# Kernel tuning notes

Hardware: AMD Instinct MI355X
Metric: run time of the kernel (lower is better)

The kernel has to match this reference:

```python
import jax, jax.numpy as jnp
import numpy as np

N_VIDEOS = 256
EMBED_DIM = 1024
MARGIN = 0.0

def _segment_sizes():
    i = np.arange(N_VIDEOS)
    num_clips = 8 + (i % 17)            # sum = 4088
    num_caps = 8 + ((5 * i + 3) % 17)   # sum = 4091
    return num_clips, num_caps

def setup_inputs() -> dict:
    key = jax.random.key(0)
    num_clips, num_caps = _segment_sizes()
    total_clips = int(num_clips.sum())
    total_caps = int(num_caps.sum())
    k1, k2 = jax.random.split(key)
    im = jax.random.normal(k1, (total_clips, EMBED_DIM), dtype=jnp.float32)
    s = jax.random.normal(k2, (total_caps, EMBED_DIM), dtype=jnp.float32)
    return {
        "im": im,
        "s": s,
        "num_clips": jnp.asarray(num_clips, jnp.int32),
        "num_caps": jnp.asarray(num_caps, jnp.int32),
    }

def reference(im, s, num_clips, num_caps):
    N = num_clips.shape[0]
    # full similarity matrix [total_clips, total_caps]
    scores = im @ s.T
    # segment ids mapping each clip/caption row to its video group
    clip_seg = jnp.repeat(jnp.arange(N), num_clips, total_repeat_length=im.shape[0])
    cap_seg = jnp.repeat(jnp.arange(N), num_caps, total_repeat_length=s.shape[0])
    # two-stage segmented sum -> block sums [N, N], then divide for block means
    row_red = jax.ops.segment_sum(scores, clip_seg, num_segments=N)       # [N, total_caps]
    blk_sum = jax.ops.segment_sum(row_red.T, cap_seg, num_segments=N).T   # [N, N]
    counts = num_clips.astype(jnp.float32)[:, None] * num_caps.astype(jnp.float32)[None, :]
    S = blk_sum / counts
    diag = jnp.diag(S)
    cost_s = jnp.maximum(MARGIN + S - diag[:, None], 0.0)   # caption retrieval
    cost_im = jnp.maximum(MARGIN + S - diag[None, :], 0.0)  # image retrieval
    eye = jnp.eye(N, dtype=bool)
    cost_s = jnp.where(eye, 0.0, cost_s)
    cost_im = jnp.where(eye, 0.0, cost_im)
    return cost_s.sum() + cost_im.sum()
```

## Files before the change

### kernel.cpp

```cpp
#include <hip/hip_runtime.h>
#include <hip/hip_bf16.h>

#define NVID 256
#define DIM 1024

typedef short bf16x8 __attribute__((ext_vector_type(8)));
typedef float f32x4 __attribute__((ext_vector_type(4)));

__device__ inline void acc4(float4& a, const float4& v) {
    a.x += v.x; a.y += v.y; a.z += v.z; a.w += v.w;
}

__device__ inline unsigned short f2bf(float f) {
    __hip_bfloat16 h = __float2bfloat16(f);
    unsigned short u;
    __builtin_memcpy(&u, &h, 2);
    return u;
}

__device__ inline float bf2f(unsigned short u) {
    return __uint_as_float(((unsigned)u) << 16);
}

__device__ inline float4 mean_rows(const float* __restrict__ src, int off, int n, int t) {
    const float4* srcv = (const float4*)src + (size_t)off * (DIM / 4) + t;
    float4 a0 = {0,0,0,0}, a1 = {0,0,0,0}, a2 = {0,0,0,0}, a3 = {0,0,0,0};
    int r = 0;
    for (; r + 8 <= n; r += 8) {
        float4 v0 = srcv[(size_t)(r + 0) * (DIM / 4)];
        float4 v1 = srcv[(size_t)(r + 1) * (DIM / 4)];
        float4 v2 = srcv[(size_t)(r + 2) * (DIM / 4)];
        float4 v3 = srcv[(size_t)(r + 3) * (DIM / 4)];
        float4 v4 = srcv[(size_t)(r + 4) * (DIM / 4)];
        float4 v5 = srcv[(size_t)(r + 5) * (DIM / 4)];
        float4 v6 = srcv[(size_t)(r + 6) * (DIM / 4)];
        float4 v7 = srcv[(size_t)(r + 7) * (DIM / 4)];
        acc4(a0, v0); acc4(a1, v1); acc4(a2, v2); acc4(a3, v3);
        acc4(a0, v4); acc4(a1, v5); acc4(a2, v6); acc4(a3, v7);
    }
    for (; r < n; ++r) acc4(a0, srcv[(size_t)r * (DIM / 4)]);
    acc4(a0, a1); acc4(a2, a3); acc4(a0, a2);
    const float inv = 1.0f / (float)n;
    a0.x *= inv; a0.y *= inv; a0.z *= inv; a0.w *= inv;
    return a0;
}

__global__ __launch_bounds__(256) void mean_diag_kernel(
    const float* __restrict__ im, const float* __restrict__ s,
    const int* __restrict__ num_clips, const int* __restrict__ num_caps,
    unsigned short* __restrict__ Ab, unsigned short* __restrict__ Bb,
    float* __restrict__ diag, float* __restrict__ out)
{
    const int i = blockIdx.x;
    const int t = threadIdx.x;
    if (i == 0 && t == 0) out[0] = 0.0f;

    __shared__ int sc[NVID], sp[NVID];
    sc[t] = num_clips[t];
    sp[t] = num_caps[t];
    __syncthreads();

    int offc = 0, offp = 0;
    for (int k = 0; k < i; ++k) { offc += sc[k]; offp += sp[k]; }
    const int nc = sc[i], np = sp[i];

    float4 am = mean_rows(im, offc, nc, t);
    float4 bm = mean_rows(s,  offp, np, t);

    ushort4 ua, ub;
    ua.x = f2bf(am.x); ua.y = f2bf(am.y); ua.z = f2bf(am.z); ua.w = f2bf(am.w);
    ub.x = f2bf(bm.x); ub.y = f2bf(bm.y); ub.z = f2bf(bm.z); ub.w = f2bf(bm.w);
    ((ushort4*)(Ab + (size_t)i * DIM))[t] = ua;
    ((ushort4*)(Bb + (size_t)i * DIM))[t] = ub;

    float p = bf2f(ua.x) * bf2f(ub.x) + bf2f(ua.y) * bf2f(ub.y)
            + bf2f(ua.z) * bf2f(ub.z) + bf2f(ua.w) * bf2f(ub.w);
    for (int o = 32; o > 0; o >>= 1) p += __shfl_down(p, o, 64);

    __shared__ float wsum[4];
    const int wave = t >> 6, lane = t & 63;
    if (lane == 0) wsum[wave] = p;
    __syncthreads();
    if (t == 0) diag[i] = wsum[0] + wsum[1] + wsum[2] + wsum[3];
}

__global__ __launch_bounds__(64) void loss_kernel(
    const unsigned short* __restrict__ Ab, const unsigned short* __restrict__ Bb,
    const float* __restrict__ diag, float* __restrict__ out)
{
    const int lane = threadIdx.x;
    const int i0 = blockIdx.y * 16, j0 = blockIdx.x * 16;
    const int m = lane & 15, q = lane >> 4;

    const unsigned short* Ap = Ab + (size_t)(i0 + m) * DIM + q * 8;
    const unsigned short* Bp = Bb + (size_t)(j0 + m) * DIM + q * 8;

    f32x4 acc = {0.f, 0.f, 0.f, 0.f};
#pragma unroll
    for (int kb = 0; kb < DIM; kb += 32) {
        bf16x8 a = *(const bf16x8*)(Ap + kb);
        bf16x8 b = *(const bf16x8*)(Bp + kb);
        acc = __builtin_amdgcn_mfma_f32_16x16x32_bf16(a, b, acc, 0, 0, 0);
    }

    const int j = j0 + m;
    const float dj = diag[j];
    const float4 di = *(const float4*)&diag[i0 + q * 4];
    const float dia[4] = {di.x, di.y, di.z, di.w};

    float v = 0.f;
#pragma unroll
    for (int r = 0; r < 4; ++r) {
        const int i = i0 + q * 4 + r;
        if (i != j) {
            const float sv = acc[r];
            v += fmaxf(sv - dia[r], 0.f) + fmaxf(sv - dj, 0.f);
        }
    }

    for (int o = 32; o > 0; o >>= 1) v += __shfl_down(v, o, 64);
    if (lane == 0) atomicAdd(out, v);
}

extern "C" void kernel_launch(void* const* d_in, const int* in_sizes, int n_in,
                              void* d_out, int out_size, void* d_ws, size_t ws_size,
                              hipStream_t stream) {
    const float* im    = (const float*)d_in[0];
    const float* s     = (const float*)d_in[1];
    const int*   nclip = (const int*)d_in[2];
    const int*   ncap  = (const int*)d_in[3];
    float* out = (float*)d_out;

    unsigned short* Ab = (unsigned short*)d_ws;
    unsigned short* Bb = Ab + NVID * DIM;
    float* diag = (float*)(Bb + NVID * DIM);

    mean_diag_kernel<<<NVID, 256, 0, stream>>>(im, s, nclip, ncap, Ab, Bb, diag, out);
    loss_kernel<<<dim3(16, 16), 64, 0, stream>>>(Ab, Bb, diag, out);
}
```

Before: 86.33 us.

## Split mean kernel across column halves and compute offsets via wave reduction

The mean/diag kernel now launches two blocks of 128 threads per video, each covering half of the embedding columns, so twice as many blocks spread across the CUs. The serial per-thread prefix loop over segment counts is replaced by a packed clip/caption count sum using a shuffle reduction. The diagonal is written as two partial sums that the loss kernel adds together. The packed 16-bit offsets assume the totals fit in 16 bits, which holds for these sizes.

```diff
diff --git a/kernel.cpp b/kernel.cpp
--- a/kernel.cpp
+++ b/kernel.cpp
@@ -22,8 +22,8 @@
     return __uint_as_float(((unsigned)u) << 16);
 }
 
-__device__ inline float4 mean_rows(const float* __restrict__ src, int off, int n, int t) {
-    const float4* srcv = (const float4*)src + (size_t)off * (DIM / 4) + t;
+__device__ inline float4 mean_rows_half(const float* __restrict__ src, int n, int t) {
+    const float4* srcv = (const float4*)src + t;
     float4 a0 = {0,0,0,0}, a1 = {0,0,0,0}, a2 = {0,0,0,0}, a3 = {0,0,0,0};
     int r = 0;
     for (; r + 8 <= n; r += 8) {
@@ -45,48 +45,60 @@
     return a0;
 }
 
-__global__ __launch_bounds__(256) void mean_diag_kernel(
+__global__ __launch_bounds__(128) void mean_diag_kernel(
     const float* __restrict__ im, const float* __restrict__ s,
     const int* __restrict__ num_clips, const int* __restrict__ num_caps,
     unsigned short* __restrict__ Ab, unsigned short* __restrict__ Bb,
-    float* __restrict__ diag, float* __restrict__ out)
+    float* __restrict__ diagp, float* __restrict__ out)
 {
-    const int i = blockIdx.x;
+    const int b = blockIdx.x;
     const int t = threadIdx.x;
-    if (i == 0 && t == 0) out[0] = 0.0f;
+    const int vid = b & (NVID - 1);
+    const int half = b >> 8;
+    if (b == 0 && t == 0) out[0] = 0.0f;
 
-    __shared__ int sc[NVID], sp[NVID];
-    sc[t] = num_clips[t];
-    sp[t] = num_caps[t];
+    int psum = 0;
+    {
+        int k0 = t, k1 = t + 128;
+        int v0 = num_clips[k0] | (num_caps[k0] << 16);
+        int v1 = num_clips[k1] | (num_caps[k1] << 16);
+        if (k0 < vid) psum += v0;
+        if (k1 < vid) psum += v1;
+    }
+    for (int o = 32; o > 0; o >>= 1) psum += __shfl_down(psum, o, 64);
+    __shared__ int wpart[2];
+    const int wave = t >> 6, lane = t & 63;
+    if (lane == 0) wpart[wave] = psum;
     __syncthreads();
+    const int packed = wpart[0] + wpart[1];
+    const int offc = packed & 0xFFFF;
+    const int offp = (packed >> 16) & 0xFFFF;
+    const int nc = num_clips[vid];
+    const int np = num_caps[vid];
 
-    int offc = 0, offp = 0;
-    for (int k = 0; k < i; ++k) { offc += sc[k]; offp += sp[k]; }
-    const int nc = sc[i], np = sp[i];
+    const int colBase = half * (DIM / 2);
 
-    float4 am = mean_rows(im, offc, nc, t);
-    float4 bm = mean_rows(s,  offp, np, t);
+    float4 am = mean_rows_half(im + (size_t)offc * DIM + colBase, nc, t);
+    float4 bm = mean_rows_half(s  + (size_t)offp * DIM + colBase, np, t);
 
     ushort4 ua, ub;
     ua.x = f2bf(am.x); ua.y = f2bf(am.y); ua.z = f2bf(am.z); ua.w = f2bf(am.w);
     ub.x = f2bf(bm.x); ub.y = f2bf(bm.y); ub.z = f2bf(bm.z); ub.w = f2bf(bm.w);
-    ((ushort4*)(Ab + (size_t)i * DIM))[t] = ua;
-    ((ushort4*)(Bb + (size_t)i * DIM))[t] = ub;
+    ((ushort4*)(Ab + (size_t)vid * DIM + colBase))[t] = ua;
+    ((ushort4*)(Bb + (size_t)vid * DIM + colBase))[t] = ub;
 
     float p = bf2f(ua.x) * bf2f(ub.x) + bf2f(ua.y) * bf2f(ub.y)
             + bf2f(ua.z) * bf2f(ub.z) + bf2f(ua.w) * bf2f(ub.w);
     for (int o = 32; o > 0; o >>= 1) p += __shfl_down(p, o, 64);
-
-    __shared__ float wsum[4];
-    const int wave = t >> 6, lane = t & 63;
+    __shared__ float wsum[2];
     if (lane == 0) wsum[wave] = p;
     __syncthreads();
-    if (t == 0) diag[i] = wsum[0] + wsum[1] + wsum[2] + wsum[3];
+    if (t == 0) diagp[half * NVID + vid] = wsum[0] + wsum[1];
 }
 
 __global__ __launch_bounds__(64) void loss_kernel(
     const unsigned short* __restrict__ Ab, const unsigned short* __restrict__ Bb,
-    const float* __restrict__ diag, float* __restrict__ out)
+    const float* __restrict__ diagp, float* __restrict__ out)
 {
     const int lane = threadIdx.x;
     const int i0 = blockIdx.y * 16, j0 = blockIdx.x * 16;
@@ -104,9 +116,10 @@
     }
 
     const int j = j0 + m;
-    const float dj = diag[j];
-    const float4 di = *(const float4*)&diag[i0 + q * 4];
-    const float dia[4] = {di.x, di.y, di.z, di.w};
+    const float dj = diagp[j] + diagp[NVID + j];
+    const float4 di0 = *(const float4*)&diagp[i0 + q * 4];
+    const float4 di1 = *(const float4*)&diagp[NVID + i0 + q * 4];
+    const float dia[4] = {di0.x + di1.x, di0.y + di1.y, di0.z + di1.z, di0.w + di1.w};
 
     float v = 0.f;
 #pragma unroll
@@ -133,8 +146,8 @@
 
     unsigned short* Ab = (unsigned short*)d_ws;
     unsigned short* Bb = Ab + NVID * DIM;
-    float* diag = (float*)(Bb + NVID * DIM);
+    float* diagp = (float*)(Bb + NVID * DIM);
 
-    mean_diag_kernel<<<NVID, 256, 0, stream>>>(im, s, nclip, ncap, Ab, Bb, diag, out);
-    loss_kernel<<<dim3(16, 16), 64, 0, stream>>>(Ab, Bb, diag, out);
+    mean_diag_kernel<<<2 * NVID, 128, 0, stream>>>(im, s, nclip, ncap, Ab, Bb, diagp, out);
+    loss_kernel<<<dim3(16, 16), 64, 0, stream>>>(Ab, Bb, diagp, out);
 }
```

New measurement: 86.52 us. About the same (+0.2%).
